# Optimization experiments

Hardware: AMD Instinct MI355X
Metric: run time of the kernel (lower is better)

## Reference

```python
import jax, jax.numpy as jnp
import numpy as np

D_MODEL = 1024
N_HEADS = 16
HEAD_DIM = D_MODEL // N_HEADS
LENGTHS = np.array([1536, 1024, 1400, 900, 1200, 1300, 1500, 1000])
OFFSETS = np.concatenate([[0], np.cumsum(LENGTHS)]).astype(np.int32)
N_TOT = int(OFFSETS[-1])
LN_EPS = 1e-5


def _pad_meta(offsets):
    # Static (numpy) gather indices: ragged concat [N,D] -> padded [B,Lmax,D]
    offsets = np.asarray(offsets)
    lengths = np.diff(offsets)
    lmax = int(lengths.max())
    tok = np.arange(lmax)[None, :]                      # [1, Lmax]
    valid = tok < lengths[:, None]                      # [B, Lmax] bool
    src = np.where(valid, offsets[:-1, None] + tok, 0)  # [B, Lmax] int
    return src, valid


def setup_inputs() -> dict:
    key = jax.random.key(0)
    ks = jax.random.split(key, 4)
    s = 1.0 / np.sqrt(D_MODEL)
    return {
        "x": jax.random.normal(ks[0], (N_TOT, D_MODEL), jnp.float32),
        "batch_offsets": jnp.asarray(OFFSETS, jnp.int32),
        "in_proj_w": jax.random.normal(ks[1], (3 * D_MODEL, D_MODEL), jnp.float32) * s,
        "in_proj_b": jnp.zeros((3 * D_MODEL,), jnp.float32),
        "out_w": jax.random.normal(ks[2], (D_MODEL, D_MODEL), jnp.float32) * s,
        "out_b": jnp.zeros((D_MODEL,), jnp.float32),
        "ln_g": jnp.ones((D_MODEL,), jnp.float32),
        "ln_b": jnp.zeros((D_MODEL,), jnp.float32),
    }


def reference(x, batch_offsets, in_proj_w, in_proj_b, out_w, out_b, ln_g, ln_b):
    src, valid = _pad_meta(np.asarray(batch_offsets))
    B, L = valid.shape
    vmask = jnp.asarray(valid)
    # deconcat_add_batch_dim: pad to [B, L, D]
    xp = x[src] * vmask[..., None]
    # pre-LayerNorm
    mu = jnp.mean(xp, axis=-1, keepdims=True)
    var = jnp.mean((xp - mu) ** 2, axis=-1, keepdims=True)
    h = (xp - mu) * jax.lax.rsqrt(var + LN_EPS) * ln_g + ln_b
    # fused qkv projection (torch MHA in_proj)
    qkv = h @ in_proj_w.T + in_proj_b                   # [B, L, 3D]
    q, k, v = jnp.split(qkv, 3, axis=-1)
    def heads(t):
        return t.reshape(B, L, N_HEADS, HEAD_DIM).transpose(0, 2, 1, 3)
    q, k, v = heads(q), heads(k), heads(v)              # [B, H, L, hd]
    scores = jnp.einsum("bhqd,bhkd->bhqk", q, k) / np.sqrt(HEAD_DIM)
    scores = jnp.where(vmask[:, None, None, :], scores, -jnp.inf)
    attn = jax.nn.softmax(scores, axis=-1)
    o = jnp.einsum("bhqk,bhkd->bhqd", attn, v)          # [B, H, L, hd]
    o = o.transpose(0, 2, 1, 3).reshape(B, L, D_MODEL)
    o = o @ out_w.T + out_b
    y = xp + o                                          # residual (dropout p=0)
    # remove_batch_dim_and_concat: unpad back to [N, D]
    return y[vmask]
```

## Files before the change

kernel.cpp:

```cpp
#include <hip/hip_runtime.h>
#include <hip/hip_bf16.h>
#include <stdint.h>

#define D_MODEL 1024
#define QKV_LD  3072
#define N_TOT   9860
#define M_PAD   9984
#define LN_EPS  1e-5f

typedef __bf16 bf16_t;
typedef __bf16 bf16x8 __attribute__((ext_vector_type(8)));
typedef float  f32x4  __attribute__((ext_vector_type(4)));

__device__ inline unsigned short f2bf(float f) {
  __bf16 h = (__bf16)f;
  return __builtin_bit_cast(unsigned short, h);
}
__device__ inline int imin(int a, int b) { return a < b ? a : b; }

__device__ inline void gload_lds16(const bf16_t* g, void* l) {
  __builtin_amdgcn_global_load_lds(
      (const __attribute__((address_space(1))) unsigned int*)g,
      (__attribute__((address_space(3))) unsigned int*)l, 16, 0, 0);
}

__global__ __launch_bounds__(256) void cvt_weights(const float* __restrict__ w_in,
                                                   const float* __restrict__ w_out,
                                                   bf16_t* __restrict__ win,
                                                   bf16_t* __restrict__ wout) {
  const int n_in = QKV_LD * D_MODEL / 4;
  int i = blockIdx.x * 256 + threadIdx.x;
  const float* src;
  ushort4* dst;
  int j;
  if (i < n_in) { src = w_in; dst = (ushort4*)win; j = i; }
  else          { src = w_out; dst = (ushort4*)wout; j = i - n_in; }
  float4 v = ((const float4*)src)[j];
  dst[j] = make_ushort4(f2bf(v.x), f2bf(v.y), f2bf(v.z), f2bf(v.w));
}

__global__ __launch_bounds__(256) void ln_kernel(const float* __restrict__ x,
                                                 const float* __restrict__ g,
                                                 const float* __restrict__ b,
                                                 bf16_t* __restrict__ hout) {
  int row = blockIdx.x;
  int t = threadIdx.x;
  if (row >= N_TOT) {
    ((ushort4*)(hout + (size_t)row * D_MODEL))[t] = make_ushort4(0, 0, 0, 0);
    return;
  }
  float4 v = ((const float4*)(x + (size_t)row * D_MODEL))[t];
  float s  = v.x + v.y + v.z + v.w;
  float sq = v.x * v.x + v.y * v.y + v.z * v.z + v.w * v.w;
  #pragma unroll
  for (int off = 1; off < 64; off <<= 1) {
    s  += __shfl_xor(s, off);
    sq += __shfl_xor(sq, off);
  }
  __shared__ float ss[4], ssq[4];
  int wid = t >> 6;
  if ((t & 63) == 0) { ss[wid] = s; ssq[wid] = sq; }
  __syncthreads();
  s  = ss[0] + ss[1] + ss[2] + ss[3];
  sq = ssq[0] + ssq[1] + ssq[2] + ssq[3];
  float mu  = s * (1.0f / 1024.0f);
  float var = sq * (1.0f / 1024.0f) - mu * mu;
  float rs  = rsqrtf(var + LN_EPS);
  float4 gv = ((const float4*)g)[t];
  float4 bv = ((const float4*)b)[t];
  ushort4 o;
  o.x = f2bf((v.x - mu) * rs * gv.x + bv.x);
  o.y = f2bf((v.y - mu) * rs * gv.y + bv.y);
  o.z = f2bf((v.z - mu) * rs * gv.z + bv.z);
  o.w = f2bf((v.w - mu) * rs * gv.w + bv.w);
  ((ushort4*)(hout + (size_t)row * D_MODEL))[t] = o;
}

template<int NCOLS, bool FINAL>
__global__ __launch_bounds__(256) void gemm_bt(const bf16_t* __restrict__ A,
                                               const bf16_t* __restrict__ B,
                                               const float* __restrict__ bias,
                                               bf16_t* __restrict__ Cbf,
                                               float* __restrict__ Cf,
                                               const float* __restrict__ resid) {
  constexpr int K = 1024;
  constexpr int GX = M_PAD / 128;
  constexpr int NWG = GX * (NCOLS / 128);
  int bid = blockIdx.x;
  bid = (bid & 7) * (NWG / 8) + (bid >> 3);
  const int tileM = bid % GX;
  const int tileN = bid / GX;
  const int t = threadIdx.x;
  const int lane = t & 63, wid = t >> 6;
  const int wr = wid >> 1, wc = wid & 1;

  __shared__ bf16_t Asm[128 * 64];
  __shared__ bf16_t Bsm[128 * 64];

  f32x4 acc[4][4];
  #pragma unroll
  for (int m = 0; m < 4; ++m)
    #pragma unroll
    for (int n = 0; n < 4; ++n)
      acc[m][n] = f32x4{0.f, 0.f, 0.f, 0.f};

  const int rowA0 = tileM * 128, rowB0 = tileN * 128;
  const int lrow = lane >> 3;
  const int lch  = lane & 7;

  for (int kt = 0; kt < K / 64; ++kt) {
    __syncthreads();
    const int k0 = kt * 64;
    #pragma unroll
    for (int i = 0; i < 4; ++i) {
      const int r  = wid * 32 + i * 8 + lrow;
      const int sc = lch ^ (r & 7);
      gload_lds16(A + (size_t)(rowA0 + r) * K + k0 + sc * 8,
                  (char*)Asm + (wid * 32 + i * 8) * 128);
      gload_lds16(B + (size_t)(rowB0 + r) * K + k0 + sc * 8,
                  (char*)Bsm + (wid * 32 + i * 8) * 128);
    }
    __syncthreads();
    #pragma unroll
    for (int ks = 0; ks < 2; ++ks) {
      bf16x8 af[4], bfr[4];
      #pragma unroll
      for (int m = 0; m < 4; ++m) {
        int r = wr * 64 + m * 16 + (lane & 15);
        int c = ks * 4 + (lane >> 4);
        af[m] = *(const bf16x8*)((const char*)Asm + r * 128 + ((c ^ (r & 7)) * 16));
      }
      #pragma unroll
      for (int n = 0; n < 4; ++n) {
        int r = wc * 64 + n * 16 + (lane & 15);
        int c = ks * 4 + (lane >> 4);
        bfr[n] = *(const bf16x8*)((const char*)Bsm + r * 128 + ((c ^ (r & 7)) * 16));
      }
      #pragma unroll
      for (int m = 0; m < 4; ++m)
        #pragma unroll
        for (int n = 0; n < 4; ++n)
          acc[m][n] = __builtin_amdgcn_mfma_f32_16x16x32_bf16(af[m], bfr[n], acc[m][n], 0, 0, 0);
    }
  }

  #pragma unroll
  for (int m = 0; m < 4; ++m) {
    int rb = tileM * 128 + wr * 64 + m * 16 + ((lane >> 4) << 2);
    #pragma unroll
    for (int n = 0; n < 4; ++n) {
      int cb = tileN * 128 + wc * 64 + n * 16 + (lane & 15);
      float bv = bias[cb];
      #pragma unroll
      for (int j = 0; j < 4; ++j) {
        int grow = rb + j;
        float val = acc[m][n][j] + bv;
        if constexpr (FINAL) {
          if (grow < N_TOT) {
            size_t idx = (size_t)grow * NCOLS + cb;
            Cf[idx] = resid[idx] + val;
          }
        } else {
          Cbf[(size_t)grow * NCOLS + cb] = (bf16_t)val;
        }
      }
    }
  }
}

__global__ __launch_bounds__(256) void transpose_v(const bf16_t* __restrict__ qkv,
                                                   bf16_t* __restrict__ vt) {
  __shared__ bf16_t tile[64][72];
  const int t = threadIdx.x;
  const int n0 = blockIdx.x * 64, c0 = blockIdx.y * 64;
  #pragma unroll
  for (int it = 0; it < 2; ++it) {
    int idx = it * 256 + t;
    int row = idx >> 3, ch = idx & 7;
    bf16x8 v = *(const bf16x8*)(qkv + (size_t)(n0 + row) * QKV_LD + 2048 + c0 + ch * 8);
    *(bf16x8*)(&tile[row][ch * 8]) = v;
  }
  __syncthreads();
  #pragma unroll
  for (int it = 0; it < 2; ++it) {
    int idx = it * 256 + t;
    int crow = idx >> 3, ng = idx & 7;
    bf16x8 o;
    #pragma unroll
    for (int i = 0; i < 8; ++i) o[i] = tile[ng * 8 + i][crow];
    *(bf16x8*)(vt + (size_t)(c0 + crow) * M_PAD + n0 + ng * 8) = o;
  }
}

__global__ __launch_bounds__(256) void attn_mfma(const bf16_t* __restrict__ qkv,
                                                 const bf16_t* __restrict__ vt,
                                                 bf16_t* __restrict__ obuf) {
  static const int off0_[8] = {0, 7360, 2560, 6060, 4860, 1536, 8860, 3960};
  static const int len_[8]  = {1536, 1500, 1400, 1300, 1200, 1024, 1000, 900};
  static const int ts_[9]   = {0, 24, 48, 70, 91, 110, 126, 142, 157};
  const int tt = blockIdx.x;
  const int h  = blockIdx.y;
  int b = 0;
  #pragma unroll
  for (int i = 1; i < 8; ++i) b += (tt >= ts_[i]);
  const int L     = len_[b];
  const int kbase = off0_[b];
  const int q0    = (tt - ts_[b]) * 64;
  const int tok0  = kbase + q0;
  const int nq    = imin(L - q0, 64);

  const int t = threadIdx.x;
  const int lane = t & 63, w = t >> 6;
  const int lg = lane >> 4, lr = lane & 15;

  __shared__ char Ks[8192];
  __shared__ char Vs[8192];
  __shared__ char Ps[8192];

  bf16x8 qf[2];
  {
    const bf16_t* qp = qkv + (size_t)(tok0 + w * 16 + lr) * QKV_LD + h * 64;
    #pragma unroll
    for (int ks = 0; ks < 2; ++ks) {
      bf16x8 v = *(const bf16x8*)(qp + ks * 32 + lg * 8);
      #pragma unroll
      for (int i = 0; i < 8; ++i) v[i] = (__bf16)((float)v[i] * 0.125f);
      qf[ks] = v;
    }
  }

  f32x4 accO[4];
  #pragma unroll
  for (int n = 0; n < 4; ++n) accO[n] = f32x4{0.f, 0.f, 0.f, 0.f};
  float m_r  = -INFINITY;
  float lsum = 0.f;

  const int srow0 = t >> 3, sch = t & 7;
  const int prow  = w * 16 + lr;

  int4 kreg[2];
  int2 vreg[2][2];
  auto load_tile = [&](int kv0) {
    #pragma unroll
    for (int it = 0; it < 2; ++it) {
      int row = srow0 + it * 32;
      kreg[it] = *(const int4*)(qkv + (size_t)(kbase + kv0 + row) * QKV_LD + 1024 + h * 64 + sch * 8);
      const bf16_t* vp = vt + (size_t)(h * 64 + row) * M_PAD + kbase + kv0 + sch * 8;
      vreg[it][0] = *(const int2*)vp;
      vreg[it][1] = *(const int2*)(vp + 4);
    }
  };

  load_tile(0);

  for (int kv0 = 0; kv0 < L; kv0 += 64) {
    const int nk = imin(L - kv0, 64);
    __syncthreads();
    #pragma unroll
    for (int it = 0; it < 2; ++it) {
      int row = srow0 + it * 32;
      int sw = ((sch ^ (row & 7)) * 16);
      *(int4*)(Ks + row * 128 + sw) = kreg[it];
      int4 vv;
      vv.x = vreg[it][0].x; vv.y = vreg[it][0].y;
      vv.z = vreg[it][1].x; vv.w = vreg[it][1].y;
      *(int4*)(Vs + row * 128 + sw) = vv;
    }
    __syncthreads();
    if (kv0 + 64 < L) load_tile(kv0 + 64);

    f32x4 accS[4];
    #pragma unroll
    for (int n = 0; n < 4; ++n) accS[n] = f32x4{0.f, 0.f, 0.f, 0.f};
    __builtin_amdgcn_s_setprio(1);
    #pragma unroll
    for (int ks = 0; ks < 2; ++ks) {
      #pragma unroll
      for (int n = 0; n < 4; ++n) {
        int key = n * 16 + lr;
        bf16x8 kf = *(const bf16x8*)(Ks + key * 128 + (((ks * 4 + lg) ^ (key & 7)) * 16));
        accS[n] = __builtin_amdgcn_mfma_f32_16x16x32_bf16(kf, qf[ks], accS[n], 0, 0, 0);
      }
    }
    __builtin_amdgcn_s_setprio(0);

    if (nk < 64) {
      #pragma unroll
      for (int n = 0; n < 4; ++n)
        #pragma unroll
        for (int r = 0; r < 4; ++r)
          if (16 * n + lg * 4 + r >= nk) accS[n][r] = -INFINITY;
    }

    float mx = accS[0][0];
    #pragma unroll
    for (int n = 0; n < 4; ++n)
      #pragma unroll
      for (int r = 0; r < 4; ++r)
        mx = fmaxf(mx, accS[n][r]);
    mx = fmaxf(mx, __shfl_xor(mx, 16));
    mx = fmaxf(mx, __shfl_xor(mx, 32));

    if (!__all(mx <= m_r + 8.0f)) {
      float mnew = fmaxf(m_r, mx);
      float scl  = __expf(m_r - mnew);
      lsum *= scl;
      #pragma unroll
      for (int j = 0; j < 4; ++j) {
        float sj = __shfl(scl, lg * 4 + j);
        #pragma unroll
        for (int n = 0; n < 4; ++n) accO[n][j] *= sj;
      }
      m_r = mnew;
    }

    #pragma unroll
    for (int n = 0; n < 4; ++n) {
      float p0 = __expf(accS[n][0] - m_r);
      float p1 = __expf(accS[n][1] - m_r);
      float p2 = __expf(accS[n][2] - m_r);
      float p3 = __expf(accS[n][3] - m_r);
      lsum += (p0 + p1) + (p2 + p3);
      uint32_t lo = (uint32_t)f2bf(p0) | ((uint32_t)f2bf(p1) << 16);
      uint32_t hi = (uint32_t)f2bf(p2) | ((uint32_t)f2bf(p3) << 16);
      int c = 2 * n + (lg >> 1);
      *(uint2*)(Ps + prow * 128 + (((c ^ (prow & 7)) * 16)) + (lg & 1) * 8) =
          make_uint2(lo, hi);
    }

    __builtin_amdgcn_s_setprio(1);
    #pragma unroll
    for (int ks = 0; ks < 2; ++ks) {
      bf16x8 pa = *(const bf16x8*)(Ps + prow * 128 + (((ks * 4 + lg) ^ (prow & 7)) * 16));
      #pragma unroll
      for (int n = 0; n < 4; ++n) {
        int dim = n * 16 + lr;
        bf16x8 vf = *(const bf16x8*)(Vs + dim * 128 + (((ks * 4 + lg) ^ (dim & 7)) * 16));
        accO[n] = __builtin_amdgcn_mfma_f32_16x16x32_bf16(pa, vf, accO[n], 0, 0, 0);
      }
    }
    __builtin_amdgcn_s_setprio(0);
  }

  float l = lsum;
  l += __shfl_xor(l, 16);
  l += __shfl_xor(l, 32);
  #pragma unroll
  for (int j = 0; j < 4; ++j) {
    float lj = __shfl(l, lg * 4 + j);
    int qlocal = w * 16 + lg * 4 + j;
    if (qlocal < nq) {
      float inv = 1.f / lj;
      bf16_t* op = obuf + (size_t)(tok0 + qlocal) * D_MODEL + h * 64;
      #pragma unroll
      for (int n = 0; n < 4; ++n)
        op[n * 16 + lr] = (bf16_t)(accO[n][j] * inv);
    }
  }
}

extern "C" void kernel_launch(void* const* d_in, const int* in_sizes, int n_in,
                              void* d_out, int out_size, void* d_ws, size_t ws_size,
                              hipStream_t stream) {
  const float* x     = (const float*)d_in[0];
  const float* w_in  = (const float*)d_in[2];
  const float* b_in  = (const float*)d_in[3];
  const float* w_out = (const float*)d_in[4];
  const float* b_out = (const float*)d_in[5];
  const float* ln_g  = (const float*)d_in[6];
  const float* ln_b  = (const float*)d_in[7];
  float* out = (float*)d_out;

  char* ws = (char*)d_ws;
  const size_t SZ_H   = (size_t)M_PAD * D_MODEL * 2;
  const size_t SZ_QKV = (size_t)M_PAD * QKV_LD * 2;
  const size_t SZ_O   = SZ_H;
  const size_t SZ_WIN = (size_t)QKV_LD * D_MODEL * 2;
  const size_t SZ_WO  = (size_t)D_MODEL * D_MODEL * 2;
  if (ws_size < SZ_H + SZ_QKV + SZ_O + SZ_WIN + SZ_WO) return;

  bf16_t* h_bf    = (bf16_t*)ws;
  bf16_t* qkv_bf  = (bf16_t*)(ws + SZ_H);
  bf16_t* o_bf    = (bf16_t*)(ws + SZ_H + SZ_QKV);
  bf16_t* win_bf  = (bf16_t*)(ws + SZ_H + SZ_QKV + SZ_O);
  bf16_t* wout_bf = (bf16_t*)(ws + SZ_H + SZ_QKV + SZ_O + SZ_WIN);

  cvt_weights<<<(QKV_LD * D_MODEL / 4 + D_MODEL * D_MODEL / 4) / 256, 256, 0, stream>>>(
      w_in, w_out, win_bf, wout_bf);

  ln_kernel<<<M_PAD, 256, 0, stream>>>(x, ln_g, ln_b, h_bf);

  gemm_bt<QKV_LD, false><<<(M_PAD / 128) * (QKV_LD / 128), 256, 0, stream>>>(
      h_bf, win_bf, b_in, qkv_bf, nullptr, nullptr);

  bf16_t* vt = h_bf;
  transpose_v<<<dim3(M_PAD / 64, D_MODEL / 64), 256, 0, stream>>>(qkv_bf, vt);

  attn_mfma<<<dim3(157, 16), 256, 0, stream>>>(qkv_bf, vt, o_bf);

  gemm_bt<D_MODEL, true><<<(M_PAD / 128) * (D_MODEL / 128), 256, 0, stream>>>(
      o_bf, wout_bf, b_out, nullptr, out, x);
}
```

Measured before the change: 346.7 us.

## Switch attention to 32x32x16 MFMA with 128-query tiles and register P

Rewrites the attention kernel to use 32x32x16 bf16 MFMAs with each wave owning 32 queries, doubling the query tile per block to 128 and halving the grid. The softmax probabilities are kept in registers and rearranged with v_permlane32_swap so they feed the PV MFMA directly, removing the P round-trip through shared memory. Because the S accumulator is transposed (keys as rows, queries as columns), each query's row max and rescale need only one cross-lane exchange instead of per-row shuffles, and output stores become vectorized. The trade-off is fewer blocks (1280 vs 2512), which lowers occupancy and load balance across the ragged sequences, plus more registers per thread.

```diff
diff --git a/kernel.cpp b/kernel.cpp
--- a/kernel.cpp
+++ b/kernel.cpp
@@ -11,12 +11,18 @@
 typedef __bf16 bf16_t;
 typedef __bf16 bf16x8 __attribute__((ext_vector_type(8)));
 typedef float  f32x4  __attribute__((ext_vector_type(4)));
+typedef float  f32x16 __attribute__((ext_vector_type(16)));
+typedef uint32_t u32x4 __attribute__((ext_vector_type(4)));
 
 __device__ inline unsigned short f2bf(float f) {
   __bf16 h = (__bf16)f;
   return __builtin_bit_cast(unsigned short, h);
 }
 __device__ inline int imin(int a, int b) { return a < b ? a : b; }
+
+__device__ inline void plswap(uint32_t& a, uint32_t& b) {
+  asm("v_permlane32_swap_b32 %0, %1" : "+v"(a), "+v"(b));
+}
 
 __device__ inline void gload_lds16(const bf16_t* g, void* l) {
   __builtin_amdgcn_global_load_lds(
@@ -197,7 +203,7 @@
                                                  bf16_t* __restrict__ obuf) {
   static const int off0_[8] = {0, 7360, 2560, 6060, 4860, 1536, 8860, 3960};
   static const int len_[8]  = {1536, 1500, 1400, 1300, 1200, 1024, 1000, 900};
-  static const int ts_[9]   = {0, 24, 48, 70, 91, 110, 126, 142, 157};
+  static const int ts_[9]   = {0, 12, 24, 35, 46, 56, 64, 72, 80};
   const int tt = blockIdx.x;
   const int h  = blockIdx.y;
   int b = 0;
@@ -205,38 +211,38 @@
   for (int i = 1; i < 8; ++i) b += (tt >= ts_[i]);
   const int L     = len_[b];
   const int kbase = off0_[b];
-  const int q0    = (tt - ts_[b]) * 64;
+  const int q0    = (tt - ts_[b]) * 128;
   const int tok0  = kbase + q0;
-  const int nq    = imin(L - q0, 64);
+  const int nq    = imin(L - q0, 128);
 
   const int t = threadIdx.x;
   const int lane = t & 63, w = t >> 6;
-  const int lg = lane >> 4, lr = lane & 15;
+  const int qcol = lane & 31, hi = lane >> 5;
 
   __shared__ char Ks[8192];
   __shared__ char Vs[8192];
-  __shared__ char Ps[8192];
-
-  bf16x8 qf[2];
+
+  bf16x8 qf[4];
   {
-    const bf16_t* qp = qkv + (size_t)(tok0 + w * 16 + lr) * QKV_LD + h * 64;
-    #pragma unroll
-    for (int ks = 0; ks < 2; ++ks) {
-      bf16x8 v = *(const bf16x8*)(qp + ks * 32 + lg * 8);
+    const bf16_t* qp = qkv + (size_t)(tok0 + w * 32 + qcol) * QKV_LD + h * 64;
+    #pragma unroll
+    for (int c = 0; c < 4; ++c) {
+      bf16x8 v = *(const bf16x8*)(qp + c * 16 + hi * 8);
       #pragma unroll
       for (int i = 0; i < 8; ++i) v[i] = (__bf16)((float)v[i] * 0.125f);
-      qf[ks] = v;
-    }
-  }
-
-  f32x4 accO[4];
-  #pragma unroll
-  for (int n = 0; n < 4; ++n) accO[n] = f32x4{0.f, 0.f, 0.f, 0.f};
+      qf[c] = v;
+    }
+  }
+
+  f32x16 accO[2];
+  #pragma unroll
+  for (int db = 0; db < 2; ++db)
+    #pragma unroll
+    for (int i = 0; i < 16; ++i) accO[db][i] = 0.f;
   float m_r  = -INFINITY;
   float lsum = 0.f;
 
   const int srow0 = t >> 3, sch = t & 7;
-  const int prow  = w * 16 + lr;
 
   int4 kreg[2];
   int2 vreg[2][2];
@@ -269,36 +275,36 @@
     __syncthreads();
     if (kv0 + 64 < L) load_tile(kv0 + 64);
 
-    f32x4 accS[4];
-    #pragma unroll
-    for (int n = 0; n < 4; ++n) accS[n] = f32x4{0.f, 0.f, 0.f, 0.f};
+    f32x16 accS[2];
+    #pragma unroll
+    for (int kb = 0; kb < 2; ++kb)
+      #pragma unroll
+      for (int i = 0; i < 16; ++i) accS[kb][i] = 0.f;
     __builtin_amdgcn_s_setprio(1);
     #pragma unroll
-    for (int ks = 0; ks < 2; ++ks) {
-      #pragma unroll
-      for (int n = 0; n < 4; ++n) {
-        int key = n * 16 + lr;
-        bf16x8 kf = *(const bf16x8*)(Ks + key * 128 + (((ks * 4 + lg) ^ (key & 7)) * 16));
-        accS[n] = __builtin_amdgcn_mfma_f32_16x16x32_bf16(kf, qf[ks], accS[n], 0, 0, 0);
+    for (int kb = 0; kb < 2; ++kb) {
+      int key = kb * 32 + qcol;
+      #pragma unroll
+      for (int c = 0; c < 4; ++c) {
+        bf16x8 kf = *(const bf16x8*)(Ks + key * 128 + (((2 * c + hi) ^ (key & 7)) * 16));
+        accS[kb] = __builtin_amdgcn_mfma_f32_32x32x16_bf16(kf, qf[c], accS[kb], 0, 0, 0);
       }
     }
     __builtin_amdgcn_s_setprio(0);
 
     if (nk < 64) {
       #pragma unroll
-      for (int n = 0; n < 4; ++n)
+      for (int kb = 0; kb < 2; ++kb)
         #pragma unroll
-        for (int r = 0; r < 4; ++r)
-          if (16 * n + lg * 4 + r >= nk) accS[n][r] = -INFINITY;
+        for (int r = 0; r < 16; ++r)
+          if (kb * 32 + (r & 3) + 8 * (r >> 2) + 4 * hi >= nk) accS[kb][r] = -INFINITY;
     }
 
     float mx = accS[0][0];
     #pragma unroll
-    for (int n = 0; n < 4; ++n)
-      #pragma unroll
-      for (int r = 0; r < 4; ++r)
-        mx = fmaxf(mx, accS[n][r]);
-    mx = fmaxf(mx, __shfl_xor(mx, 16));
+    for (int r = 1; r < 16; ++r) mx = fmaxf(mx, accS[0][r]);
+    #pragma unroll
+    for (int r = 0; r < 16; ++r) mx = fmaxf(mx, accS[1][r]);
     mx = fmaxf(mx, __shfl_xor(mx, 32));
 
     if (!__all(mx <= m_r + 8.0f)) {
@@ -306,56 +312,71 @@
       float scl  = __expf(m_r - mnew);
       lsum *= scl;
       #pragma unroll
+      for (int db = 0; db < 2; ++db)
+        #pragma unroll
+        for (int i = 0; i < 16; ++i) accO[db][i] *= scl;
+      m_r = mnew;
+    }
+
+    bf16x8 pb[2][2];
+    #pragma unroll
+    for (int kb = 0; kb < 2; ++kb) {
+      uint32_t G[4][2];
+      #pragma unroll
       for (int j = 0; j < 4; ++j) {
-        float sj = __shfl(scl, lg * 4 + j);
+        float p0 = __expf(accS[kb][4 * j + 0] - m_r);
+        float p1 = __expf(accS[kb][4 * j + 1] - m_r);
+        float p2 = __expf(accS[kb][4 * j + 2] - m_r);
+        float p3 = __expf(accS[kb][4 * j + 3] - m_r);
+        lsum += (p0 + p1) + (p2 + p3);
+        G[j][0] = (uint32_t)f2bf(p0) | ((uint32_t)f2bf(p1) << 16);
+        G[j][1] = (uint32_t)f2bf(p2) | ((uint32_t)f2bf(p3) << 16);
+      }
+      #pragma unroll
+      for (int c = 0; c < 2; ++c) {
+        uint32_t ax = G[2 * c][0], bx = G[2 * c + 1][0];
+        uint32_t ay = G[2 * c][1], by = G[2 * c + 1][1];
+        plswap(ax, bx);
+        plswap(ay, by);
+        u32x4 u; u[0] = ax; u[1] = ay; u[2] = bx; u[3] = by;
+        pb[kb][c] = __builtin_bit_cast(bf16x8, u);
+      }
+    }
+
+    __builtin_amdgcn_s_setprio(1);
+    #pragma unroll
+    for (int kb = 0; kb < 2; ++kb)
+      #pragma unroll
+      for (int c = 0; c < 2; ++c) {
+        int ch = 4 * kb + 2 * c + hi;
         #pragma unroll
-        for (int n = 0; n < 4; ++n) accO[n][j] *= sj;
-      }
-      m_r = mnew;
-    }
-
-    #pragma unroll
-    for (int n = 0; n < 4; ++n) {
-      float p0 = __expf(accS[n][0] - m_r);
-      float p1 = __expf(accS[n][1] - m_r);
-      float p2 = __expf(accS[n][2] - m_r);
-      float p3 = __expf(accS[n][3] - m_r);
-      lsum += (p0 + p1) + (p2 + p3);
-      uint32_t lo = (uint32_t)f2bf(p0) | ((uint32_t)f2bf(p1) << 16);
-      uint32_t hi = (uint32_t)f2bf(p2) | ((uint32_t)f2bf(p3) << 16);
-      int c = 2 * n + (lg >> 1);
-      *(uint2*)(Ps + prow * 128 + (((c ^ (prow & 7)) * 16)) + (lg & 1) * 8) =
-          make_uint2(lo, hi);
-    }
-
-    __builtin_amdgcn_s_setprio(1);
-    #pragma unroll
-    for (int ks = 0; ks < 2; ++ks) {
-      bf16x8 pa = *(const bf16x8*)(Ps + prow * 128 + (((ks * 4 + lg) ^ (prow & 7)) * 16));
-      #pragma unroll
-      for (int n = 0; n < 4; ++n) {
-        int dim = n * 16 + lr;
-        bf16x8 vf = *(const bf16x8*)(Vs + dim * 128 + (((ks * 4 + lg) ^ (dim & 7)) * 16));
-        accO[n] = __builtin_amdgcn_mfma_f32_16x16x32_bf16(pa, vf, accO[n], 0, 0, 0);
-      }
-    }
+        for (int db = 0; db < 2; ++db) {
+          int dim = db * 32 + qcol;
+          bf16x8 vf = *(const bf16x8*)(Vs + dim * 128 + ((ch ^ (dim & 7)) * 16));
+          accO[db] = __builtin_amdgcn_mfma_f32_32x32x16_bf16(vf, pb[kb][c], accO[db], 0, 0, 0);
+        }
+      }
     __builtin_amdgcn_s_setprio(0);
   }
 
-  float l = lsum;
-  l += __shfl_xor(l, 16);
-  l += __shfl_xor(l, 32);
-  #pragma unroll
-  for (int j = 0; j < 4; ++j) {
-    float lj = __shfl(l, lg * 4 + j);
-    int qlocal = w * 16 + lg * 4 + j;
-    if (qlocal < nq) {
-      float inv = 1.f / lj;
-      bf16_t* op = obuf + (size_t)(tok0 + qlocal) * D_MODEL + h * 64;
-      #pragma unroll
-      for (int n = 0; n < 4; ++n)
-        op[n * 16 + lr] = (bf16_t)(accO[n][j] * inv);
-    }
+  float l = lsum + __shfl_xor(lsum, 32);
+  const int qlocal = w * 32 + qcol;
+  if (qlocal < nq) {
+    float inv = 1.f / l;
+    bf16_t* op = obuf + (size_t)(tok0 + qlocal) * D_MODEL + h * 64;
+    #pragma unroll
+    for (int db = 0; db < 2; ++db)
+      #pragma unroll
+      for (int rr = 0; rr < 4; ++rr) {
+        float v0 = accO[db][4 * rr + 0] * inv;
+        float v1 = accO[db][4 * rr + 1] * inv;
+        float v2 = accO[db][4 * rr + 2] * inv;
+        float v3 = accO[db][4 * rr + 3] * inv;
+        uint2 u;
+        u.x = (uint32_t)f2bf(v0) | ((uint32_t)f2bf(v1) << 16);
+        u.y = (uint32_t)f2bf(v2) | ((uint32_t)f2bf(v3) << 16);
+        *(uint2*)(op + db * 32 + rr * 8 + hi * 4) = u;
+      }
   }
 }
 
@@ -396,7 +417,7 @@
   bf16_t* vt = h_bf;
   transpose_v<<<dim3(M_PAD / 64, D_MODEL / 64), 256, 0, stream>>>(qkv_bf, vt);
 
-  attn_mfma<<<dim3(157, 16), 256, 0, stream>>>(qkv_bf, vt, o_bf);
+  attn_mfma<<<dim3(80, 16), 256, 0, stream>>>(qkv_bf, vt, o_bf);
 
   gemm_bt<D_MODEL, true><<<(M_PAD / 128) * (D_MODEL / 128), 256, 0, stream>>>(
       o_bf, wout_bf, b_out, nullptr, out, x);
```

New measurement: 335.5 us. -3.2%, faster.
